# Kernel tuning notes

Measured on AMD Instinct MI355X. Metric: run time of the kernel, lower is better.

## Reference

```python
import jax, jax.numpy as jnp
import numpy as np

N_NODES, N_EDGES, N_GRAPHS, NUM_FEATURES, NUM_CLASSES = 100000, 1600000, 512, 128, 10
EPS = 1e-5


def gat_conv(x, W, a_src, a_dst, b, src, dst, heads, out_ch):
    # PyG GATConv: h = xW -> [N,H,C]; per-node scores; leaky_relu; segment softmax over dst; scatter-add
    N = x.shape[0]
    h = (x @ W).reshape(N, heads, out_ch)
    s_src = jnp.einsum('nhc,hc->nh', h, a_src)
    s_dst = jnp.einsum('nhc,hc->nh', h, a_dst)
    score = jax.nn.leaky_relu(s_src[src] + s_dst[dst], 0.2)          # [E,H]
    m = jax.ops.segment_max(score, dst, num_segments=N)              # stable softmax per dst node
    e = jnp.exp(score - m[dst])
    denom = jax.ops.segment_sum(e, dst, num_segments=N)
    alpha = e / denom[dst]                                            # self-loops guarantee denom>0
    out = jax.ops.segment_sum(alpha[:, :, None] * h[src], dst, num_segments=N)
    return out.reshape(N, heads * out_ch) + b


def batch_norm(x, g, b):
    mu = x.mean(0)
    var = x.var(0)  # biased, as torch BN uses for normalization
    return g * (x - mu) * jax.lax.rsqrt(var + EPS) + b


def setup_inputs() -> dict:
    key = jax.random.key(0)
    ks = jax.random.split(key, 32)
    r = lambda i, shape: jax.random.normal(ks[i], shape, dtype=jnp.float32) * 0.1
    inp = {
        'x': jax.random.normal(ks[0], (N_NODES, NUM_FEATURES), dtype=jnp.float32),
        'edge_index': jax.random.randint(ks[1], (2, N_EDGES), 0, N_NODES, dtype=jnp.int64),
        'batch': jnp.sort(jax.random.randint(ks[2], (N_NODES,), 0, N_GRAPHS, dtype=jnp.int64)),
        # conv1: 128 -> 8 ch x 8 heads
        'W1': r(3, (NUM_FEATURES, 64)), 'a1s': r(4, (8, 8)), 'a1d': r(5, (8, 8)), 'b1': r(6, (64,)),
        'g1': jnp.ones(64), 'be1': jnp.zeros(64),
        'lW1': r(7, (64, 8)), 'lb1': r(8, (8,)), 'gl1': jnp.ones(8), 'bel1': jnp.zeros(8),
        # conv2: 8 -> 16 ch x 4 heads
        'W2': r(9, (8, 64)), 'a2s': r(10, (4, 16)), 'a2d': r(11, (4, 16)), 'b2': r(12, (64,)),
        'g2': jnp.ones(64), 'be2': jnp.zeros(64),
        'lW2': r(13, (64, 16)), 'lb2': r(14, (16,)), 'gl2': jnp.ones(16), 'bel2': jnp.zeros(16),
        # conv3: 16 -> 24 ch x 4 heads
        'W3': r(15, (16, 96)), 'a3s': r(16, (4, 24)), 'a3d': r(17, (4, 24)), 'b3': r(18, (96,)),
        'g3': jnp.ones(96), 'be3': jnp.zeros(96),
        'oW': r(19, (96, NUM_CLASSES)), 'ob': r(20, (NUM_CLASSES,)),
    }
    return inp


def reference(x, edge_index, batch, W1, a1s, a1d, b1, g1, be1, lW1, lb1, gl1, bel1,
              W2, a2s, a2d, b2, g2, be2, lW2, lb2, gl2, bel2,
              W3, a3s, a3d, b3, g3, be3, oW, ob):
    N = x.shape[0]
    loops = jnp.arange(N, dtype=edge_index.dtype)
    src = jnp.concatenate([edge_index[0], loops])  # PyG add_self_loops default
    dst = jnp.concatenate([edge_index[1], loops])

    h = gat_conv(x, W1, a1s, a1d, b1, src, dst, 8, 8)
    h = jax.nn.relu(batch_norm(h, g1, be1))
    h = jax.nn.relu(batch_norm(h @ lW1 + lb1, gl1, bel1))

    h = gat_conv(h, W2, a2s, a2d, b2, src, dst, 4, 16)
    h = jax.nn.relu(batch_norm(h, g2, be2))
    h = jax.nn.relu(batch_norm(h @ lW2 + lb2, gl2, bel2))

    h = gat_conv(h, W3, a3s, a3d, b3, src, dst, 4, 24)
    h = jax.nn.relu(batch_norm(h, g3, be3))

    sums = jax.ops.segment_sum(h, batch, num_segments=N_GRAPHS)
    cnts = jax.ops.segment_sum(jnp.ones((N,), h.dtype), batch, num_segments=N_GRAPHS)
    pooled = sums / jnp.maximum(cnts, 1.0)[:, None]
    return pooled @ oW + ob
```

## Files before the change

### kernel.cpp

```cpp
#include <hip/hip_runtime.h>
#include <hip/hip_fp16.h>
#include <math.h>

#define NN 100000
#define NE 1600000
#define ET (NE + NN)
#define NG 512
#define STATS_BLOCKS 240
#define SCAN_B 1024
#define SCAN_NB ((NN + SCAN_B - 1) / SCAN_B)
#define PSLOTS (ET + 7 * NN)

#define BSH 9
#define NB  ((NN + 511) / 512)
#define BCAP 12288
#define CHUNK 4096


__global__ __launch_bounds__(256) void part_pass1(const int* __restrict__ ei,
                                                  int* __restrict__ bcur,
                                                  unsigned* __restrict__ pairs) {
    __shared__ unsigned pck[CHUNK];
    __shared__ unsigned ordv[CHUNK];
    __shared__ unsigned char bkt[CHUNK];
    __shared__ unsigned char obkt[CHUNK];
    __shared__ int hist[NB + 1];
    __shared__ int lofs[NB + 1];
    __shared__ int cur[NB + 1];
    __shared__ int gpos[NB];
    __shared__ int lh[256];

    int t = threadIdx.x;
    int base = blockIdx.x * CHUNK;
    for (int i = t; i <= NB; i += 256) hist[i] = 0;
    __syncthreads();
    for (int i = t; i < CHUNK; i += 256) {
        int e = base + i;
        int b;
        unsigned p = 0;
        if (e < ET) {
            int s, d;
            if (e < NE) { s = ei[e]; d = ei[NE + e]; }
            else        { s = d = e - NE; }
            b = d >> BSH;
            p = ((unsigned)s << BSH) | (unsigned)(d & 511);
        } else b = NB;
        bkt[i] = (unsigned char)b;
        pck[i] = p;
        atomicAdd(&hist[b], 1);
    }
    __syncthreads();
    int v = (t <= NB) ? hist[t] : 0;
    lh[t] = v;
    __syncthreads();
    for (int off = 1; off < 256; off <<= 1) {
        int x = (t >= off) ? lh[t - off] : 0;
        __syncthreads();
        lh[t] += x;
        __syncthreads();
    }
    if (t <= NB) { lofs[t] = lh[t] - v; cur[t] = lh[t] - v; }
    __syncthreads();
    if (t < NB) {
        int h = hist[t];
        gpos[t] = (h > 0) ? atomicAdd(&bcur[t], h) : 0;
    }
    __syncthreads();
    for (int i = t; i < CHUNK; i += 256) {
        int b = bkt[i];
        int pos = atomicAdd(&cur[b], 1);
        ordv[pos] = pck[i];
        obkt[pos] = (unsigned char)b;
    }
    __syncthreads();
    int nvalid = lofs[NB];
    for (int i = t; i < nvalid; i += 256) {
        int b = obkt[i];
        int dst = gpos[b] + (i - lofs[b]);
        if (dst < BCAP) pairs[(size_t)b * BCAP + dst] = ordv[i];
    }
}


__global__ __launch_bounds__(256) void bucket_counts(const unsigned* __restrict__ pairs,
                                                     const int* __restrict__ bcur,
                                                     int* __restrict__ counts) {
    __shared__ int lhist[512];
    int b = blockIdx.x;
    int t = threadIdx.x;
    for (int i = t; i < 512; i += 256) lhist[i] = 0;
    __syncthreads();
    int cnt = min(bcur[b], BCAP);
    const unsigned* seg = pairs + (size_t)b * BCAP;
    for (int i = t; i < cnt; i += 256)
        atomicAdd(&lhist[seg[i] & 511], 1);
    __syncthreads();
    int nbase = b << BSH;
    for (int i = t; i < 512; i += 256) {
        int n = nbase + i;
        if (n < NN) counts[n] = lhist[i];
    }
}


__global__ __launch_bounds__(256) void bucket_scatter(const unsigned* __restrict__ pairs,
                                                      const int* __restrict__ bcur,
                                                      const int* __restrict__ offsets,
                                                      int* __restrict__ srcs) {
    __shared__ int cur[512];
    int b = blockIdx.x;
    int t = threadIdx.x;
    int nbase = b << BSH;
    for (int i = t; i < 512; i += 256) {
        int n = nbase + i;
        cur[i] = (n < NN) ? offsets[n] : 0;
    }
    __syncthreads();
    int cnt = min(bcur[b], BCAP);
    const unsigned* seg = pairs + (size_t)b * BCAP;
    for (int i = t; i < cnt; i += 256) {
        unsigned p = seg[i];
        int pos = atomicAdd(&cur[p & 511], 1);
        srcs[pos] = (int)(p >> BSH);
    }
}


__global__ void graph_bounds(const int* __restrict__ batch, int* __restrict__ goff) {
    int g = blockIdx.x * blockDim.x + threadIdx.x;
    if (g > NG) return;
    int lo = 0, hi = NN;
    while (lo < hi) {
        int mid = (lo + hi) >> 1;
        if (batch[mid] < g) lo = mid + 1; else hi = mid;
    }
    goff[g] = lo;
}


__global__ void scan_reduce(const int* __restrict__ in, int* __restrict__ bsum) {
    __shared__ int lds[256];
    int b = blockIdx.x, t = threadIdx.x;
    int s = 0;
    for (int i = t; i < SCAN_B; i += 256) {
        int idx = b * SCAN_B + i;
        if (idx < NN) s += (in[idx] + 7) & ~7;
    }
    lds[t] = s;
    __syncthreads();
    for (int off = 128; off > 0; off >>= 1) {
        if (t < off) lds[t] += lds[t + off];
        __syncthreads();
    }
    if (t == 0) bsum[b] = lds[0];
}

__global__ void scan_bsums(const int* __restrict__ bsum, int nb, int* __restrict__ boff,
                           int* __restrict__ total_loc) {
    __shared__ int lds[128];
    int t = threadIdx.x;
    int v = (t < nb) ? bsum[t] : 0;
    lds[t] = v;
    __syncthreads();
    for (int off = 1; off < 128; off <<= 1) {
        int x = (t >= off) ? lds[t - off] : 0;
        __syncthreads();
        lds[t] += x;
        __syncthreads();
    }
    if (t < nb) boff[t] = lds[t] - v;
    if (t == nb - 1) {
        boff[nb] = lds[t];
        if (total_loc) *total_loc = lds[t];
    }
}

__global__ void scan_final(const int* __restrict__ in, const int* __restrict__ boff,
                           int* __restrict__ out) {
    __shared__ int lds[SCAN_B];
    int b = blockIdx.x, t = threadIdx.x;
    int idx = b * SCAN_B + t;
    int v = (idx < NN) ? ((in[idx] + 7) & ~7) : 0;
    lds[t] = v;
    __syncthreads();
    for (int off = 1; off < SCAN_B; off <<= 1) {
        int x = (t >= off) ? lds[t - off] : 0;
        __syncthreads();
        lds[t] += x;
        __syncthreads();
    }
    if (idx < NN) out[idx] = boff[b] + lds[t] - v;
}


__global__ __launch_bounds__(256) void gemm1(const float* __restrict__ X,
                                             const float* __restrict__ W,
                                             __half* __restrict__ Hh) {
    __shared__ float wl[128 * 64];
    __shared__ float xl[32 * 132];
    int t = threadIdx.x;
    int n0 = blockIdx.x * 32;
    for (int i = t * 4; i < 128 * 64; i += 1024)
        *(float4*)&wl[i] = *(const float4*)&W[i];
    for (int i = t * 4; i < 32 * 128; i += 1024) {
        int r = i >> 7, c = i & 127;
        int n = n0 + r;
        float4 v = (n < NN) ? *(const float4*)&X[(size_t)n * 128 + c] : make_float4(0, 0, 0, 0);
        *(float4*)&xl[r * 132 + c] = v;
    }
    __syncthreads();
    int cg = (t & 15) * 4;
    int ng = (t >> 4) * 2;
    float acc[2][4] = {};
    for (int k = 0; k < 128; ++k) {
        float4 w4 = *(float4*)&wl[k * 64 + cg];
        #pragma unroll
        for (int j = 0; j < 2; ++j) {
            float xv = xl[(ng + j) * 132 + k];
            acc[j][0] += xv * w4.x; acc[j][1] += xv * w4.y;
            acc[j][2] += xv * w4.z; acc[j][3] += xv * w4.w;
        }
    }
    #pragma unroll
    for (int j = 0; j < 2; ++j) {
        int n = n0 + ng + j;
        if (n < NN) {
            __half2 p0 = __floats2half2_rn(acc[j][0], acc[j][1]);
            __half2 p1 = __floats2half2_rn(acc[j][2], acc[j][3]);
            *(__half2*)&Hh[(size_t)n * 64 + cg] = p0;
            *(__half2*)&Hh[(size_t)n * 64 + cg + 2] = p1;
        }
    }
}


__global__ void scores_kernel(const __half* __restrict__ Hh, const float* __restrict__ a_s,
                              const float* __restrict__ a_d, float* __restrict__ SS,
                              float* __restrict__ SD, int HEADS, int C) {
    int idx = blockIdx.x * blockDim.x + threadIdx.x;
    if (idx >= NN * HEADS) return;
    int n = idx / HEADS, h = idx % HEADS;
    const __half* row = Hh + (size_t)n * HEADS * C + h * C;
    float s1 = 0.f, s2 = 0.f;
    for (int c = 0; c < C; c += 2) {
        float2 v = __half22float2(*(const __half2*)&row[c]);
        s1 += v.x * a_s[h * C + c] + v.y * a_s[h * C + c + 1];
        s2 += v.x * a_d[h * C + c] + v.y * a_d[h * C + c + 1];
    }
    SS[idx] = s1;
    SD[idx] = s2;
}


template <int H>
__global__ __launch_bounds__(256) void weights_kernel(const float* __restrict__ SS,
                                                      const float* __restrict__ SD,
                                                      const int* __restrict__ offsets,
                                                      const int* __restrict__ counts,
                                                      const int* __restrict__ srcs,
                                                      __half* __restrict__ w) {
    int wid = blockIdx.x * 4 + (threadIdx.x >> 6);
    if (wid >= NN) return;
    int lane = threadIdx.x & 63;
    constexpr int SPG = 64 / H;
    int so = lane / H, h = lane % H;
    int beg = offsets[wid], end = offsets[wid + 1];
    int deg = counts[wid];
    float sdv = SD[(unsigned)wid * H + h];
    for (int g = beg; g < end; g += SPG) {
        int slot = g + so;
        if (slot < end) {
            int src = srcs[slot];
            float sc = SS[(unsigned)src * H + h] + sdv;
            sc = sc > 0.f ? sc : 0.2f * sc;
            float wv = (slot - beg) < deg ? __expf(sc) : 0.f;
            w[(unsigned)slot * H + h] = __float2half(wv);
        }
    }
}


template <int HEADS, int C, int PL, int GRP>
__global__ __launch_bounds__(256) void gat_kernel(const __half* __restrict__ Hh,
                                                  const __half* __restrict__ w,
                                                  const int* __restrict__ offsets,
                                                  const int* __restrict__ srcs,
                                                  const float* __restrict__ bias,
                                                  __half* __restrict__ GO) {
    constexpr int CH = HEADS * C;
    int wid = blockIdx.x * (blockDim.x >> 6) + (threadIdx.x >> 6);
    int lane = threadIdx.x & 63;
    if (wid >= NN) return;
    int ch0 = lane * PL;
    bool active = ch0 < CH;
    int ch0l = active ? ch0 : 0;
    int head = active ? (ch0 / C) : 0;
    int beg = offsets[wid], end = offsets[wid + 1];
    float s = 0.f, a0 = 0.f, a1 = 0.f;
    int e = beg;
    if (GRP == 16) {
        for (; e + 16 <= end; e += 16) {
            int sv[16];
            float wv[16];
            #pragma unroll
            for (int i = 0; i < 16; ++i) {
                sv[i] = srcs[e + i];
                wv[i] = __half2float(w[(unsigned)(e + i) * HEADS + head]);
            }
            float hv0[16];
            #pragma unroll
            for (int i = 0; i < 16; ++i)
                hv0[i] = __half2float(Hh[(unsigned)(sv[i] * CH) + ch0l]);
            float pw[8], pa[8];
            #pragma unroll
            for (int i = 0; i < 8; ++i) {
                pw[i] = wv[2 * i] + wv[2 * i + 1];
                pa[i] = wv[2 * i] * hv0[2 * i] + wv[2 * i + 1] * hv0[2 * i + 1];
            }
            s  += ((pw[0] + pw[1]) + (pw[2] + pw[3])) + ((pw[4] + pw[5]) + (pw[6] + pw[7]));
            a0 += ((pa[0] + pa[1]) + (pa[2] + pa[3])) + ((pa[4] + pa[5]) + (pa[6] + pa[7]));
        }
    }
    for (; e < end; e += 8) {
        int sv[8];
        float wv[8];
        #pragma unroll
        for (int i = 0; i < 8; ++i) {
            sv[i] = srcs[e + i];
            wv[i] = __half2float(w[(unsigned)(e + i) * HEADS + head]);
        }
        float hv0[8], hv1[8];
        #pragma unroll
        for (int i = 0; i < 8; ++i) {
            if (PL == 2) {
                __half2 hp = *(const __half2*)&Hh[(unsigned)(sv[i] * CH) + ch0l];
                hv0[i] = __low2float(hp); hv1[i] = __high2float(hp);
            } else {
                hv0[i] = __half2float(Hh[(unsigned)(sv[i] * CH) + ch0l]);
                hv1[i] = 0.f;
            }
        }
        float ws = ((wv[0] + wv[1]) + (wv[2] + wv[3])) + ((wv[4] + wv[5]) + (wv[6] + wv[7]));
        float as0 = ((wv[0] * hv0[0] + wv[1] * hv0[1]) + (wv[2] * hv0[2] + wv[3] * hv0[3]))
                  + ((wv[4] * hv0[4] + wv[5] * hv0[5]) + (wv[6] * hv0[6] + wv[7] * hv0[7]));
        s += ws;
        a0 += as0;
        if (PL == 2) {
            float as1 = ((wv[0] * hv1[0] + wv[1] * hv1[1]) + (wv[2] * hv1[2] + wv[3] * hv1[3]))
                      + ((wv[4] * hv1[4] + wv[5] * hv1[5]) + (wv[6] * hv1[6] + wv[7] * hv1[7]));
            a1 += as1;
        }
    }
    if (active) {
        float inv = 1.f / s;
        if (PL == 2) {
            *(__half2*)&GO[(unsigned)(wid * CH) + ch0] =
                __floats2half2_rn(a0 * inv + bias[ch0], a1 * inv + bias[ch0 + 1]);
        } else {
            GO[(unsigned)(wid * CH) + ch0] = __float2half(a0 * inv + bias[ch0]);
        }
    }
}


__global__ void stats_kernel(const float* __restrict__ X, int Nn, int C,
                             float* __restrict__ partial) {
    int t = threadIdx.x;
    int c = t % C;
    int grp = t / C;
    int G_ = blockDim.x / C;
    float s = 0.f, q = 0.f;
    for (int n = blockIdx.x * G_ + grp; n < Nn; n += gridDim.x * G_) {
        float v = X[(size_t)n * C + c];
        s += v; q += v * v;
    }
    extern __shared__ float lds[];
    lds[t] = s; lds[blockDim.x + t] = q;
    __syncthreads();
    for (int off = blockDim.x >> 1; off >= C; off >>= 1) {
        if (t < off) {
            lds[t] += lds[t + off];
            lds[blockDim.x + t] += lds[blockDim.x + t + off];
        }
        __syncthreads();
    }
    if (t < C) {
        partial[(size_t)blockIdx.x * 2 * C + t] = lds[t];
        partial[(size_t)blockIdx.x * 2 * C + C + t] = lds[blockDim.x + t];
    }
}

__global__ void stats_h_kernel(const __half* __restrict__ X, int Nn, int C,
                               float* __restrict__ partial) {
    int t = threadIdx.x;
    int c = t % C;
    int grp = t / C;
    int G_ = blockDim.x / C;
    float s = 0.f, q = 0.f;
    for (int n = blockIdx.x * G_ + grp; n < Nn; n += gridDim.x * G_) {
        float v = __half2float(X[(size_t)n * C + c]);
        s += v; q += v * v;
    }
    extern __shared__ float lds[];
    lds[t] = s; lds[blockDim.x + t] = q;
    __syncthreads();
    for (int off = blockDim.x >> 1; off >= C; off >>= 1) {
        if (t < off) {
            lds[t] += lds[t + off];
            lds[blockDim.x + t] += lds[blockDim.x + t + off];
        }
        __syncthreads();
    }
    if (t < C) {
        partial[(size_t)blockIdx.x * 2 * C + t] = lds[t];
        partial[(size_t)blockIdx.x * 2 * C + C + t] = lds[blockDim.x + t];
    }
}

__global__ void bn_finalize(const float* __restrict__ partial, int nb, int C, float invN,
                            const float* __restrict__ g, const float* __restrict__ be,
                            float* __restrict__ scale, float* __restrict__ shift) {
    extern __shared__ float red[];
    int t = threadIdx.x;
    int c = t % C;
    int grp = t / C;
    int G_ = blockDim.x / C;
    float s = 0.f, q = 0.f;
    for (int b = grp; b < nb; b += G_) {
        s += partial[(size_t)b * 2 * C + c];
        q += partial[(size_t)b * 2 * C + C + c];
    }
    red[t] = s; red[blockDim.x + t] = q;
    __syncthreads();
    for (int off = blockDim.x >> 1; off >= C; off >>= 1) {
        if (t < off) {
            red[t] += red[t + off];
            red[blockDim.x + t] += red[blockDim.x + t + off];
        }
        __syncthreads();
    }
    if (t < C) {
        float mean = red[t] * invN;
        float var = fmaxf(red[blockDim.x + t] * invN - mean * mean, 0.f);
        float rs = rsqrtf(var + 1e-5f);
        float sc = g[t] * rs;
        scale[t] = sc;
        shift[t] = be[t] - mean * sc;
    }
}


template <int KOUT>
__global__ __launch_bounds__(256) void bnrelu_linear(const __half* __restrict__ X,
                                                     const float* __restrict__ scale,
                                                     const float* __restrict__ shift,
                                                     const float* __restrict__ Lw,
                                                     const float* __restrict__ lb,
                                                     float* __restrict__ U) {
    __shared__ float tl[64 * 65];
    int t = threadIdx.x;
    int n0 = blockIdx.x * 64;
    for (int i = t * 4; i < 64 * 64; i += 1024) {
        int r = i >> 6, cc = i & 63;
        int n = n0 + r;
        float vv[4] = {0.f, 0.f, 0.f, 0.f};
        if (n < NN) {
            float2 v0 = __half22float2(*(const __half2*)&X[(size_t)n * 64 + cc]);
            float2 v1 = __half22float2(*(const __half2*)&X[(size_t)n * 64 + cc + 2]);
            vv[0] = v0.x; vv[1] = v0.y; vv[2] = v1.x; vv[3] = v1.y;
        }
        #pragma unroll
        for (int j = 0; j < 4; ++j)
            tl[r * 65 + cc + j] = fmaxf(vv[j] * scale[cc + j] + shift[cc + j], 0.f);
    }
    __syncthreads();
    int nl = t & 63;
    int kg = (t >> 6) * (KOUT / 4);
    float acc[KOUT / 4] = {};
    for (int l = 0; l < 64; ++l) {
        float v = tl[nl * 65 + l];
        #pragma unroll
        for (int j = 0; j < KOUT / 4; ++j) acc[j] += v * Lw[l * KOUT + kg + j];
    }
    int n = n0 + nl;
    if (n < NN)
        #pragma unroll
        for (int j = 0; j < KOUT / 4; ++j)
            U[(size_t)n * KOUT + kg + j] = acc[j] + lb[kg + j];
}


template <int CIN, int COUT>
__global__ __launch_bounds__(256) void bnrelu_gemm(const float* __restrict__ U,
                                                   const float* __restrict__ scale,
                                                   const float* __restrict__ shift,
                                                   const float* __restrict__ W,
                                                   __half* __restrict__ Hh) {
    int t = threadIdx.x;
    int nl = t >> 2;
    int q = t & 3;
    int n = blockIdx.x * 64 + nl;
    if (n >= NN) return;
    constexpr int CPT = COUT / 4;
    float v[CIN];
    #pragma unroll
    for (int c = 0; c < CIN; ++c)
        v[c] = fmaxf(U[(size_t)n * CIN + c] * scale[c] + shift[c], 0.f);
    float acc[CPT] = {};
    #pragma unroll
    for (int c = 0; c < CIN; ++c) {
        #pragma unroll
        for (int j = 0; j < CPT; ++j) acc[j] += v[c] * W[c * COUT + q * CPT + j];
    }
    #pragma unroll
    for (int j = 0; j < CPT; j += 2)
        *(__half2*)&Hh[(size_t)n * COUT + q * CPT + j] = __floats2half2_rn(acc[j], acc[j + 1]);
}


__global__ __launch_bounds__(256) void pool_kernel(const __half* __restrict__ GO,
                                                   const float* __restrict__ scale,
                                                   const float* __restrict__ shift,
                                                   const int* __restrict__ goff,
                                                   float* __restrict__ pooled) {
    __shared__ float red[8][32];
    int g = blockIdx.x;
    int ch = blockIdx.y * 32 + (threadIdx.x & 31);
    int row = threadIdx.x >> 5;
    int beg = goff[g], end = goff[g + 1];
    float sc = scale[ch], sh = shift[ch];
    float s = 0.f;
    for (int n = beg + row; n < end; n += 8)
        s += fmaxf(__half2float(GO[(size_t)n * 96 + ch]) * sc + sh, 0.f);
    red[row][threadIdx.x & 31] = s;
    __syncthreads();
    if (row == 0) {
        #pragma unroll
        for (int r = 1; r < 8; ++r) s += red[r][threadIdx.x & 31];
        float cnt = (float)(end - beg);
        pooled[g * 96 + ch] = s / fmaxf(cnt, 1.f);
    }
}

__global__ void final_gemm(const float* __restrict__ pooled, const float* __restrict__ oW,
                           const float* __restrict__ ob, float* __restrict__ out) {
    int idx = blockIdx.x * blockDim.x + threadIdx.x;
    if (idx >= NG * 10) return;
    int g = idx / 10, k = idx % 10;
    float s = ob[k];
    for (int c = 0; c < 96; ++c) s += pooled[g * 96 + c] * oW[c * 10 + k];
    out[idx] = s;
}


extern "C" void kernel_launch(void* const* d_in, const int* in_sizes, int n_in,
                              void* d_out, int out_size, void* d_ws, size_t ws_size,
                              hipStream_t stream) {
    const float* x   = (const float*)d_in[0];
    const int*   ei  = (const int*)d_in[1];
    const int*   bat = (const int*)d_in[2];
    const float *W1 = (const float*)d_in[3], *a1s = (const float*)d_in[4],
                *a1d = (const float*)d_in[5], *b1 = (const float*)d_in[6],
                *g1 = (const float*)d_in[7], *be1 = (const float*)d_in[8],
                *lW1 = (const float*)d_in[9], *lb1 = (const float*)d_in[10],
                *gl1 = (const float*)d_in[11], *bel1 = (const float*)d_in[12],
                *W2 = (const float*)d_in[13], *a2s = (const float*)d_in[14],
                *a2d = (const float*)d_in[15], *b2 = (const float*)d_in[16],
                *g2 = (const float*)d_in[17], *be2 = (const float*)d_in[18],
                *lW2 = (const float*)d_in[19], *lb2 = (const float*)d_in[20],
                *gl2 = (const float*)d_in[21], *bel2 = (const float*)d_in[22],
                *W3 = (const float*)d_in[23], *a3s = (const float*)d_in[24],
                *a3d = (const float*)d_in[25], *b3 = (const float*)d_in[26],
                *g3 = (const float*)d_in[27], *be3 = (const float*)d_in[28],
                *oW = (const float*)d_in[29], *ob = (const float*)d_in[30];
    float* out = (float*)d_out;

    int* iw      = (int*)d_ws;
    int* bcur    = iw;
    int* counts  = bcur + NB;
    int* offsets = counts + NN;
    int* goff    = offsets + NN + 1;
    int* bsum    = goff + NG + 1;
    int* boff    = bsum + SCAN_NB;
    int* srcs    = boff + SCAN_NB + 1;
    float* fw      = (float*)(srcs + PSLOTS);
    __half* GOh    = (__half*)fw;
    float* Ub      = fw + (size_t)NN * 96;
    float* SSb     = Ub + (size_t)NN * 16;
    float* SDb     = SSb + (size_t)NN * 8;
    float* partial = SDb + (size_t)NN * 8;
    float* scaleA  = partial + STATS_BLOCKS * 192;
    float* shiftA  = scaleA + 96;
    float* scaleB  = shiftA + 96;
    float* shiftB  = scaleB + 16;
    float* pooled  = shiftB + 16;
    __half* Hh     = (__half*)(pooled + NG * 96);
    __half* wbuf   = (__half*)(Hh + (size_t)NN * 96);
    unsigned* pairs = (unsigned*)GOh;

    const float invN = 1.0f / (float)NN;

    hipMemsetAsync(bcur, 0, NB * sizeof(int), stream);
    hipMemsetAsync(srcs, 0, (size_t)PSLOTS * sizeof(int), stream);
    part_pass1<<<(ET + CHUNK - 1) / CHUNK, 256, 0, stream>>>(ei, bcur, pairs);
    graph_bounds<<<3, 256, 0, stream>>>(bat, goff);
    bucket_counts<<<NB, 256, 0, stream>>>(pairs, bcur, counts);
    scan_reduce<<<SCAN_NB, 256, 0, stream>>>(counts, bsum);
    scan_bsums<<<1, 128, 0, stream>>>(bsum, SCAN_NB, boff, &offsets[NN]);
    scan_final<<<SCAN_NB, SCAN_B, 0, stream>>>(counts, boff, offsets);
    bucket_scatter<<<NB, 256, 0, stream>>>(pairs, bcur, offsets, srcs);

    gemm1<<<(NN + 31) / 32, 256, 0, stream>>>(x, W1, Hh);
    scores_kernel<<<(NN * 8 + 255) / 256, 256, 0, stream>>>(Hh, a1s, a1d, SSb, SDb, 8, 8);
    weights_kernel<8><<<(NN + 3) / 4, 256, 0, stream>>>(SSb, SDb, offsets, counts, srcs, wbuf);
    gat_kernel<8, 8, 1, 16><<<(NN + 3) / 4, 256, 0, stream>>>(Hh, wbuf, offsets, srcs, b1, GOh);
    stats_h_kernel<<<STATS_BLOCKS, 256, 2 * 256 * sizeof(float), stream>>>(GOh, NN, 64, partial);
    bn_finalize<<<1, 512, 2 * 512 * sizeof(float), stream>>>(partial, STATS_BLOCKS, 64, invN, g1, be1, scaleA, shiftA);
    bnrelu_linear<8><<<(NN + 63) / 64, 256, 0, stream>>>(GOh, scaleA, shiftA, lW1, lb1, Ub);
    stats_kernel<<<STATS_BLOCKS, 256, 2 * 256 * sizeof(float), stream>>>(Ub, NN, 8, partial);
    bn_finalize<<<1, 512, 2 * 512 * sizeof(float), stream>>>(partial, STATS_BLOCKS, 8, invN, gl1, bel1, scaleB, shiftB);

    bnrelu_gemm<8, 64><<<(NN + 63) / 64, 256, 0, stream>>>(Ub, scaleB, shiftB, W2, Hh);
    scores_kernel<<<(NN * 4 + 255) / 256, 256, 0, stream>>>(Hh, a2s, a2d, SSb, SDb, 4, 16);
    weights_kernel<4><<<(NN + 3) / 4, 256, 0, stream>>>(SSb, SDb, offsets, counts, srcs, wbuf);
    gat_kernel<4, 16, 1, 16><<<(NN + 3) / 4, 256, 0, stream>>>(Hh, wbuf, offsets, srcs, b2, GOh);
    stats_h_kernel<<<STATS_BLOCKS, 256, 2 * 256 * sizeof(float), stream>>>(GOh, NN, 64, partial);
    bn_finalize<<<1, 512, 2 * 512 * sizeof(float), stream>>>(partial, STATS_BLOCKS, 64, invN, g2, be2, scaleA, shiftA);
    bnrelu_linear<16><<<(NN + 63) / 64, 256, 0, stream>>>(GOh, scaleA, shiftA, lW2, lb2, Ub);
    stats_kernel<<<STATS_BLOCKS, 256, 2 * 256 * sizeof(float), stream>>>(Ub, NN, 16, partial);
    bn_finalize<<<1, 512, 2 * 512 * sizeof(float), stream>>>(partial, STATS_BLOCKS, 16, invN, gl2, bel2, scaleB, shiftB);

    bnrelu_gemm<16, 96><<<(NN + 63) / 64, 256, 0, stream>>>(Ub, scaleB, shiftB, W3, Hh);
    scores_kernel<<<(NN * 4 + 255) / 256, 256, 0, stream>>>(Hh, a3s, a3d, SSb, SDb, 4, 24);
    weights_kernel<4><<<(NN + 3) / 4, 256, 0, stream>>>(SSb, SDb, offsets, counts, srcs, wbuf);
    gat_kernel<4, 24, 2, 8><<<(NN + 3) / 4, 256, 0, stream>>>(Hh, wbuf, offsets, srcs, b3, GOh);
    stats_h_kernel<<<STATS_BLOCKS, 192, 2 * 192 * sizeof(float), stream>>>(GOh, NN, 96, partial);
    bn_finalize<<<1, 768, 2 * 768 * sizeof(float), stream>>>(partial, STATS_BLOCKS, 96, invN, g3, be3, scaleA, shiftA);

    pool_kernel<<<dim3(NG, 3), 256, 0, stream>>>(GOh, scaleA, shiftA, goff, pooled);
    final_gemm<<<(NG * 10 + 255) / 256, 256, 0, stream>>>(pooled, oW, ob, out);
}
```

Before: 693.0 us.

## Fuse attention scores into GEMMs and compute edge weights inside aggregation kernel

Per-node source/destination attention scores are now computed in the GEMM epilogues (gemm1 and bnrelu_gemm), which removes the separate scores kernel and its re-read of the half-precision features. The weights kernel that materialized per-edge exp scores into a half buffer is removed. The aggregation kernel now gathers SS per edge and computes leaky-relu and exp inline. This eliminates six launches and the write and re-read of the per-edge weight buffer, at the cost of redundant exp evaluation across the lanes that share a head and an extra per-edge gather inside the aggregation kernel.

```diff
diff --git a/kernel.cpp b/kernel.cpp
--- a/kernel.cpp
+++ b/kernel.cpp
@@ -195,7 +195,11 @@
 
 __global__ __launch_bounds__(256) void gemm1(const float* __restrict__ X,
                                              const float* __restrict__ W,
-                                             __half* __restrict__ Hh) {
+                                             const float* __restrict__ a_s,
+                                             const float* __restrict__ a_d,
+                                             __half* __restrict__ Hh,
+                                             float* __restrict__ SS,
+                                             float* __restrict__ SD) {
     __shared__ float wl[128 * 64];
     __shared__ float xl[32 * 132];
     int t = threadIdx.x;
@@ -221,60 +225,28 @@
             acc[j][2] += xv * w4.z; acc[j][3] += xv * w4.w;
         }
     }
+    int hd = cg >> 3;
+    int half = cg & 7;
     #pragma unroll
     for (int j = 0; j < 2; ++j) {
         int n = n0 + ng + j;
+        float p1 = 0.f, p2 = 0.f;
+        #pragma unroll
+        for (int k = 0; k < 4; ++k) {
+            p1 += acc[j][k] * a_s[hd * 8 + half + k];
+            p2 += acc[j][k] * a_d[hd * 8 + half + k];
+        }
+        float f1 = p1 + __shfl_xor(p1, 1, 64);
+        float f2 = p2 + __shfl_xor(p2, 1, 64);
         if (n < NN) {
-            __half2 p0 = __floats2half2_rn(acc[j][0], acc[j][1]);
-            __half2 p1 = __floats2half2_rn(acc[j][2], acc[j][3]);
-            *(__half2*)&Hh[(size_t)n * 64 + cg] = p0;
-            *(__half2*)&Hh[(size_t)n * 64 + cg + 2] = p1;
-        }
-    }
-}
-
-
-__global__ void scores_kernel(const __half* __restrict__ Hh, const float* __restrict__ a_s,
-                              const float* __restrict__ a_d, float* __restrict__ SS,
-                              float* __restrict__ SD, int HEADS, int C) {
-    int idx = blockIdx.x * blockDim.x + threadIdx.x;
-    if (idx >= NN * HEADS) return;
-    int n = idx / HEADS, h = idx % HEADS;
-    const __half* row = Hh + (size_t)n * HEADS * C + h * C;
-    float s1 = 0.f, s2 = 0.f;
-    for (int c = 0; c < C; c += 2) {
-        float2 v = __half22float2(*(const __half2*)&row[c]);
-        s1 += v.x * a_s[h * C + c] + v.y * a_s[h * C + c + 1];
-        s2 += v.x * a_d[h * C + c] + v.y * a_d[h * C + c + 1];
-    }
-    SS[idx] = s1;
-    SD[idx] = s2;
-}
-
-
-template <int H>
-__global__ __launch_bounds__(256) void weights_kernel(const float* __restrict__ SS,
-                                                      const float* __restrict__ SD,
-                                                      const int* __restrict__ offsets,
-                                                      const int* __restrict__ counts,
-                                                      const int* __restrict__ srcs,
-                                                      __half* __restrict__ w) {
-    int wid = blockIdx.x * 4 + (threadIdx.x >> 6);
-    if (wid >= NN) return;
-    int lane = threadIdx.x & 63;
-    constexpr int SPG = 64 / H;
-    int so = lane / H, h = lane % H;
-    int beg = offsets[wid], end = offsets[wid + 1];
-    int deg = counts[wid];
-    float sdv = SD[(unsigned)wid * H + h];
-    for (int g = beg; g < end; g += SPG) {
-        int slot = g + so;
-        if (slot < end) {
-            int src = srcs[slot];
-            float sc = SS[(unsigned)src * H + h] + sdv;
-            sc = sc > 0.f ? sc : 0.2f * sc;
-            float wv = (slot - beg) < deg ? __expf(sc) : 0.f;
-            w[(unsigned)slot * H + h] = __float2half(wv);
+            __half2 q0 = __floats2half2_rn(acc[j][0], acc[j][1]);
+            __half2 q1 = __floats2half2_rn(acc[j][2], acc[j][3]);
+            *(__half2*)&Hh[(size_t)n * 64 + cg] = q0;
+            *(__half2*)&Hh[(size_t)n * 64 + cg + 2] = q1;
+            if (half == 0) {
+                SS[(unsigned)n * 8 + hd] = f1;
+                SD[(unsigned)n * 8 + hd] = f2;
+            }
         }
     }
 }
@@ -282,8 +254,10 @@
 
 template <int HEADS, int C, int PL, int GRP>
 __global__ __launch_bounds__(256) void gat_kernel(const __half* __restrict__ Hh,
-                                                  const __half* __restrict__ w,
+                                                  const float* __restrict__ SS,
+                                                  const float* __restrict__ SD,
                                                   const int* __restrict__ offsets,
+                                                  const int* __restrict__ counts,
                                                   const int* __restrict__ srcs,
                                                   const float* __restrict__ bias,
                                                   __half* __restrict__ GO) {
@@ -296,6 +270,8 @@
     int ch0l = active ? ch0 : 0;
     int head = active ? (ch0 / C) : 0;
     int beg = offsets[wid], end = offsets[wid + 1];
+    int deg = counts[wid];
+    float sdv = SD[(unsigned)wid * HEADS + head];
     float s = 0.f, a0 = 0.f, a1 = 0.f;
     int e = beg;
     if (GRP == 16) {
@@ -305,7 +281,9 @@
             #pragma unroll
             for (int i = 0; i < 16; ++i) {
                 sv[i] = srcs[e + i];
-                wv[i] = __half2float(w[(unsigned)(e + i) * HEADS + head]);
+                float sc = SS[(unsigned)(sv[i] * HEADS) + head] + sdv;
+                sc = fmaxf(sc, 0.f) + 0.2f * fminf(sc, 0.f);
+                wv[i] = (e + i - beg) < deg ? __expf(sc) : 0.f;
             }
             float hv0[16];
             #pragma unroll
@@ -327,7 +305,9 @@
         #pragma unroll
         for (int i = 0; i < 8; ++i) {
             sv[i] = srcs[e + i];
-            wv[i] = __half2float(w[(unsigned)(e + i) * HEADS + head]);
+            float sc = SS[(unsigned)(sv[i] * HEADS) + head] + sdv;
+            sc = fmaxf(sc, 0.f) + 0.2f * fminf(sc, 0.f);
+            wv[i] = (e + i - beg) < deg ? __expf(sc) : 0.f;
         }
         float hv0[8], hv1[8];
         #pragma unroll
@@ -490,12 +470,17 @@
 }
 
 
-template <int CIN, int COUT>
+template <int CIN, int COUT, int H, int C>
 __global__ __launch_bounds__(256) void bnrelu_gemm(const float* __restrict__ U,
                                                    const float* __restrict__ scale,
                                                    const float* __restrict__ shift,
                                                    const float* __restrict__ W,
-                                                   __half* __restrict__ Hh) {
+                                                   const float* __restrict__ a_s,
+                                                   const float* __restrict__ a_d,
+                                                   __half* __restrict__ Hh,
+                                                   float* __restrict__ SS,
+                                                   float* __restrict__ SD) {
+    static_assert(COUT / 4 == C && H == 4, "thread-per-head mapping");
     int t = threadIdx.x;
     int nl = t >> 2;
     int q = t & 3;
@@ -512,6 +497,14 @@
         #pragma unroll
         for (int j = 0; j < CPT; ++j) acc[j] += v[c] * W[c * COUT + q * CPT + j];
     }
+    float s1 = 0.f, s2 = 0.f;
+    #pragma unroll
+    for (int j = 0; j < CPT; ++j) {
+        s1 += acc[j] * a_s[q * C + j];
+        s2 += acc[j] * a_d[q * C + j];
+    }
+    SS[(unsigned)n * H + q] = s1;
+    SD[(unsigned)n * H + q] = s2;
     #pragma unroll
     for (int j = 0; j < CPT; j += 2)
         *(__half2*)&Hh[(size_t)n * COUT + q * CPT + j] = __floats2half2_rn(acc[j], acc[j + 1]);
@@ -595,7 +588,6 @@
     float* shiftB  = scaleB + 16;
     float* pooled  = shiftB + 16;
     __half* Hh     = (__half*)(pooled + NG * 96);
-    __half* wbuf   = (__half*)(Hh + (size_t)NN * 96);
     unsigned* pairs = (unsigned*)GOh;
 
     const float invN = 1.0f / (float)NN;
@@ -610,30 +602,24 @@
     scan_final<<<SCAN_NB, SCAN_B, 0, stream>>>(counts, boff, offsets);
     bucket_scatter<<<NB, 256, 0, stream>>>(pairs, bcur, offsets, srcs);
 
-    gemm1<<<(NN + 31) / 32, 256, 0, stream>>>(x, W1, Hh);
-    scores_kernel<<<(NN * 8 + 255) / 256, 256, 0, stream>>>(Hh, a1s, a1d, SSb, SDb, 8, 8);
-    weights_kernel<8><<<(NN + 3) / 4, 256, 0, stream>>>(SSb, SDb, offsets, counts, srcs, wbuf);
-    gat_kernel<8, 8, 1, 16><<<(NN + 3) / 4, 256, 0, stream>>>(Hh, wbuf, offsets, srcs, b1, GOh);
+    gemm1<<<(NN + 31) / 32, 256, 0, stream>>>(x, W1, a1s, a1d, Hh, SSb, SDb);
+    gat_kernel<8, 8, 1, 16><<<(NN + 3) / 4, 256, 0, stream>>>(Hh, SSb, SDb, offsets, counts, srcs, b1, GOh);
     stats_h_kernel<<<STATS_BLOCKS, 256, 2 * 256 * sizeof(float), stream>>>(GOh, NN, 64, partial);
     bn_finalize<<<1, 512, 2 * 512 * sizeof(float), stream>>>(partial, STATS_BLOCKS, 64, invN, g1, be1, scaleA, shiftA);
     bnrelu_linear<8><<<(NN + 63) / 64, 256, 0, stream>>>(GOh, scaleA, shiftA, lW1, lb1, Ub);
     stats_kernel<<<STATS_BLOCKS, 256, 2 * 256 * sizeof(float), stream>>>(Ub, NN, 8, partial);
     bn_finalize<<<1, 512, 2 * 512 * sizeof(float), stream>>>(partial, STATS_BLOCKS, 8, invN, gl1, bel1, scaleB, shiftB);
 
-    bnrelu_gemm<8, 64><<<(NN + 63) / 64, 256, 0, stream>>>(Ub, scaleB, shiftB, W2, Hh);
-    scores_kernel<<<(NN * 4 + 255) / 256, 256, 0, stream>>>(Hh, a2s, a2d, SSb, SDb, 4, 16);
-    weights_kernel<4><<<(NN + 3) / 4, 256, 0, stream>>>(SSb, SDb, offsets, counts, srcs, wbuf);
-    gat_kernel<4, 16, 1, 16><<<(NN + 3) / 4, 256, 0, stream>>>(Hh, wbuf, offsets, srcs, b2, GOh);
+    bnrelu_gemm<8, 64, 4, 16><<<(NN + 63) / 64, 256, 0, stream>>>(Ub, scaleB, shiftB, W2, a2s, a2d, Hh, SSb, SDb);
+    gat_kernel<4, 16, 1, 16><<<(NN + 3) / 4, 256, 0, stream>>>(Hh, SSb, SDb, offsets, counts, srcs, b2, GOh);
     stats_h_kernel<<<STATS_BLOCKS, 256, 2 * 256 * sizeof(float), stream>>>(GOh, NN, 64, partial);
     bn_finalize<<<1, 512, 2 * 512 * sizeof(float), stream>>>(partial, STATS_BLOCKS, 64, invN, g2, be2, scaleA, shiftA);
     bnrelu_linear<16><<<(NN + 63) / 64, 256, 0, stream>>>(GOh, scaleA, shiftA, lW2, lb2, Ub);
     stats_kernel<<<STATS_BLOCKS, 256, 2 * 256 * sizeof(float), stream>>>(Ub, NN, 16, partial);
     bn_finalize<<<1, 512, 2 * 512 * sizeof(float), stream>>>(partial, STATS_BLOCKS, 16, invN, gl2, bel2, scaleB, shiftB);
 
-    bnrelu_gemm<16, 96><<<(NN + 63) / 64, 256, 0, stream>>>(Ub, scaleB, shiftB, W3, Hh);
-    scores_kernel<<<(NN * 4 + 255) / 256, 256, 0, stream>>>(Hh, a3s, a3d, SSb, SDb, 4, 24);
-    weights_kernel<4><<<(NN + 3) / 4, 256, 0, stream>>>(SSb, SDb, offsets, counts, srcs, wbuf);
-    gat_kernel<4, 24, 2, 8><<<(NN + 3) / 4, 256, 0, stream>>>(Hh, wbuf, offsets, srcs, b3, GOh);
+    bnrelu_gemm<16, 96, 4, 24><<<(NN + 63) / 64, 256, 0, stream>>>(Ub, scaleB, shiftB, W3, a3s, a3d, Hh, SSb, SDb);
+    gat_kernel<4, 24, 2, 8><<<(NN + 3) / 4, 256, 0, stream>>>(Hh, SSb, SDb, offsets, counts, srcs, b3, GOh);
     stats_h_kernel<<<STATS_BLOCKS, 192, 2 * 192 * sizeof(float), stream>>>(GOh, NN, 96, partial);
     bn_finalize<<<1, 768, 2 * 768 * sizeof(float), stream>>>(partial, STATS_BLOCKS, 96, invN, g3, be3, scaleA, shiftA);
 
```

After: 607.4 us. 1.14x faster.
